# Performance work log

Hardware: AMD Instinct MI355X
Metric: run time of the kernel (lower is better)

## Reference

```python
import jax, jax.numpy as jnp
import numpy as np

C = 16          # state channels
RATE = 0.5      # stochastic update rate
PI2 = 6.283185307179586


def _perception_kernel():
    # depthwise 3x3x3 filters: identity + sobel along each spatial axis
    g = np.array([1.0, 2.0, 1.0], np.float32)
    d = np.array([-1.0, 0.0, 1.0], np.float32)
    ident = np.zeros((3, 3, 3), np.float32); ident[1, 1, 1] = 1.0
    sx = np.einsum('i,j,k->ijk', d, g, g) / 8.0
    sy = np.einsum('i,j,k->ijk', g, d, g) / 8.0
    sz = np.einsum('i,j,k->ijk', g, g, d) / 8.0
    filt = np.stack([ident, sx, sy, sz])                 # [4,3,3,3]
    k = np.broadcast_to(filt, (C, 4, 3, 3, 3)).reshape(C * 4, 1, 3, 3, 3)
    return jnp.asarray(k)                                # [4C,1,3,3,3] OIDHW, groups=C


def _forward(x, rand_u, w1, b1, w2):
    # alive mask: 3x3x3 max-pool (stride 1, SAME) on alpha channel 3, > 0.1
    alpha = x[:, 3:4]
    pooled = jax.lax.reduce_window(alpha, -jnp.inf, jax.lax.max,
                                   (1, 1, 3, 3, 3), (1, 1, 1, 1, 1), 'SAME')
    alive = (pooled > 0.1).astype(x.dtype)               # [B,1,D,H,W]

    # anisotropic perception: depthwise stencil -> [B,4C,D,H,W]
    p = jax.lax.conv_general_dilated(
        x, _perception_kernel(), window_strides=(1, 1, 1), padding='SAME',
        dimension_numbers=('NCDHW', 'OIDHW', 'NCDHW'), feature_group_count=C)

    # per-voxel MLP (1x1x1 convs): 4C -> hidden -> C
    h = jax.nn.relu(jnp.einsum('bcxyz,oc->boxyz', p, w1)
                    + b1[None, :, None, None, None])
    upd = jnp.einsum('bcxyz,oc->boxyz', h, w2)

    # stochastic residual update + alive gating (ANISOTROPIC: 0 orientation ch.)
    smask = (rand_u <= RATE).astype(x.dtype)             # [B,1,D,H,W]
    x = x + upd * smask
    return x * alive


def setup_inputs() -> dict:
    key = jax.random.key(0)
    k1, k2, k3, k4, k5 = jax.random.split(key, 5)
    B, D = 4, 64
    H, P = 128, 4 * C
    x = jax.random.normal(k1, (B, C, D, D, D), jnp.float32)
    rand_u = jax.random.uniform(k2, (B, 1, D, D, D), jnp.float32)
    w1 = jax.random.normal(k3, (H, P), jnp.float32) * (1.0 / np.sqrt(P))
    b1 = jax.random.normal(k4, (H,), jnp.float32) * 0.01
    w2 = jax.random.normal(k5, (C, H), jnp.float32) * (1.0 / np.sqrt(H))
    return {"x": x, "rand_u": rand_u, "w1": w1, "b1": b1, "w2": w2}


def reference(x, rand_u, w1, b1, w2):
    return _forward(x, rand_u, w1, b1, w2)
```

## Files before the change

### kernel.cpp

```cpp
#include <hip/hip_runtime.h>

#define QST 600
#define NSITES 2400


typedef __attribute__((ext_vector_type(8))) short bf16x8;
typedef __attribute__((ext_vector_type(4))) float f32x4;
typedef __attribute__((ext_vector_type(2))) float f32x2;

__device__ __forceinline__ unsigned short f2bf(float f) {
    __bf16 h = (__bf16)f;
    return __builtin_bit_cast(unsigned short, h);
}
__device__ __forceinline__ unsigned packbf2(float lo, float hi) {
    return (unsigned)f2bf(lo) | ((unsigned)f2bf(hi) << 16);
}
__device__ __forceinline__ float blo(unsigned u) { return __builtin_bit_cast(float, u << 16); }
__device__ __forceinline__ float bhi(unsigned u) { return __builtin_bit_cast(float, u & 0xffff0000u); }
__device__ __forceinline__ bf16x8 pack8f(const float* s, const float* scl) {
    bf16x8 o;
    #pragma unroll
    for (int k = 0; k < 8; ++k) o[k] = (short)f2bf(s[k] * scl[k & 3]);
    return o;
}

__global__ __launch_bounds__(256) void permute_w(
    const float* __restrict__ w1, const float* __restrict__ w2,
    unsigned short* __restrict__ wsW)
{
    const int t = threadIdx.x;
    const float sclW1[4] = {1.f, 0.125f, 0.125f, 0.125f};
    const float sclId[4] = {1.f, 1.f, 1.f, 1.f};
    #pragma unroll
    for (int j = 0; j < 4; ++j) {
        int w = t + 256 * j;
        int lane = w & 63, f = (w >> 6) & 3, ch = w >> 8;
        int r16 = lane & 15, g = lane >> 4;
        int row = ch * 32 + 8 * (r16 >> 2) + (r16 & 3) + 4 * (f >> 1);
        int col = (f & 1) * 32 + g * 8;
        *(bf16x8*)(wsW + w * 8) = pack8f(w1 + row * 64 + col, sclW1);
    }
    {
        int w = t;
        int lane = w & 63, ch = w >> 6;
        int r16 = lane & 15, g = lane >> 4;
        *(bf16x8*)(wsW + 8192 + w * 8) = pack8f(w2 + r16 * 128 + ch * 32 + g * 8, sclId);
    }
}

__global__ __launch_bounds__(256, 3) void nca_fused(
    const float* __restrict__ x, const float* __restrict__ rand_u,
    const unsigned short* __restrict__ wsW, const float* __restrict__ b1,
    float* __restrict__ out)
{
    __shared__ __align__(16) char smem[51968];
    uint2*          tq = (uint2*)smem;
    unsigned short* Ps = (unsigned short*)(smem + 19200);

    const int tid = threadIdx.x;

    const int orig = blockIdx.x + 8 * blockIdx.y + 64 * blockIdx.z;
    const int work = (orig & 7) * 512 + (orig >> 3);
    const int gx0 = (work & 7) * 8;
    const int gy0 = ((work >> 3) & 7) * 8;
    const int zb  = work >> 6;
    const int b   = zb >> 4, gz0 = (zb & 15) * 4;
    const int xbase = b * (16 * 262144);

    const int tx = tid & 7, ty = (tid >> 3) & 7, tz = tid >> 6;

    const float ru = rand_u[b * 262144 + (gz0 + tz) * 4096 + (gy0 + ty) * 64 + (gx0 + tx)];

    if (tid < 240) {
        int cq = tid / 60, rem = tid - cq * 60;
        int z = rem / 10, y = rem - z * 10;
        int gz = gz0 + z - 1, gy = gy0 + y - 1;
        uint4* dst = (uint4*)(tq + cq * QST + z * 100 + y * 10);
        if ((unsigned)gz < 64u && (unsigned)gy < 64u) {
            const bool lok = (gx0 > 0), rok = (gx0 < 56);
            const float* base = x + xbase + cq * (4 * 262144) + gz * 4096 + gy * 64 + gx0;
            float va[10], vb[10];
            unsigned wlo[10], whi[10];
            #pragma unroll
            for (int half = 0; half < 2; ++half) {
                #pragma unroll
                for (int cc = 0; cc < 2; ++cc) {
                    const float* bp = base + (2 * half + cc) * 262144;
                    float* v = cc ? vb : va;
                    float4 a4 = *(const float4*)(bp);
                    float4 b4 = *(const float4*)(bp + 4);
                    v[0] = lok ? bp[-1] : 0.f;
                    v[1] = a4.x; v[2] = a4.y; v[3] = a4.z; v[4] = a4.w;
                    v[5] = b4.x; v[6] = b4.y; v[7] = b4.z; v[8] = b4.w;
                    v[9] = rok ? bp[8] : 0.f;
                }
                unsigned* wdst = half ? whi : wlo;
                #pragma unroll
                for (int k = 0; k < 10; ++k) wdst[k] = packbf2(va[k], vb[k]);
            }
            #pragma unroll
            for (int k = 0; k < 5; ++k)
                dst[k] = make_uint4(wlo[2 * k], whi[2 * k], wlo[2 * k + 1], whi[2 * k + 1]);
        } else {
            #pragma unroll
            for (int k = 0; k < 5; ++k)
                dst[k] = make_uint4(0u, 0u, 0u, 0u);
        }
    }
    __syncthreads();

    const int lane = tid & 63, wv = tid >> 6;
    const int g = lane >> 4, r16 = lane & 15;
    const int rowbase = (tz * 10 + ty) * 10 + tx;

    float pool3 = -1e30f;
    const f32x2 two = 2.f;

    #pragma unroll
    for (int cq = 0; cq < 4; ++cq) {
        uint2 q[3][3][3];
        #pragma unroll
        for (int i2 = 0; i2 < 3; ++i2)
            #pragma unroll
            for (int j = 0; j < 3; ++j) {
                const uint2* rp = tq + cq * QST + i2 * 100 + j * 10 + rowbase;
                q[i2][j][0] = rp[0]; q[i2][j][1] = rp[1]; q[i2][j][2] = rp[2];
            }

        f32x2 s1p[2], s2p[2], s3p[2];
        uint2 idq = q[1][1][1];
        #pragma unroll
        for (int pr = 0; pr < 2; ++pr) { s1p[pr] = 0.f; s2p[pr] = 0.f; s3p[pr] = 0.f; }

        #pragma unroll
        for (int i2 = 0; i2 < 3; ++i2) {
            f32x2 Ap[2], Bp[2], Cp[2];
            #pragma unroll
            for (int pr = 0; pr < 2; ++pr) { Ap[pr] = 0.f; Bp[pr] = 0.f; Cp[pr] = 0.f; }
            #pragma unroll
            for (int j = 0; j < 3; ++j) {
                uint2 q0 = q[i2][j][0], q1 = q[i2][j][1], q2 = q[i2][j][2];
                f32x2 v0[2] = { {blo(q0.x), bhi(q0.x)}, {blo(q0.y), bhi(q0.y)} };
                f32x2 v1[2] = { {blo(q1.x), bhi(q1.x)}, {blo(q1.y), bhi(q1.y)} };
                f32x2 v2[2] = { {blo(q2.x), bhi(q2.x)}, {blo(q2.y), bhi(q2.y)} };
                if (cq == 0)
                    pool3 = fmaxf(pool3, fmaxf(fmaxf(v0[1].y, v1[1].y), v2[1].y));
                #pragma unroll
                for (int pr = 0; pr < 2; ++pr) {
                    f32x2 rg = __builtin_elementwise_fma(two, v1[pr], v0[pr] + v2[pr]);
                    f32x2 rd = v2[pr] - v0[pr];
                    if (j == 1) {
                        Ap[pr] = __builtin_elementwise_fma(two, rg, Ap[pr]);
                        Cp[pr] = __builtin_elementwise_fma(two, rd, Cp[pr]);
                    } else {
                        Ap[pr] = Ap[pr] + rg;
                        Cp[pr] = Cp[pr] + rd;
                        if (j == 0) Bp[pr] = Bp[pr] - rg;
                        else        Bp[pr] = Bp[pr] + rg;
                    }
                }
            }
            #pragma unroll
            for (int pr = 0; pr < 2; ++pr) {
                if (i2 == 0) {
                    s1p[pr] = s1p[pr] - Ap[pr];
                    s2p[pr] = s2p[pr] + Bp[pr];
                    s3p[pr] = s3p[pr] + Cp[pr];
                } else if (i2 == 1) {
                    s2p[pr] = __builtin_elementwise_fma(two, Bp[pr], s2p[pr]);
                    s3p[pr] = __builtin_elementwise_fma(two, Cp[pr], s3p[pr]);
                } else {
                    s1p[pr] = s1p[pr] + Ap[pr];
                    s2p[pr] = s2p[pr] + Bp[pr];
                    s3p[pr] = s3p[pr] + Cp[pr];
                }
            }
        }
        unsigned short ide[4] = {
            (unsigned short)(idq.x & 0xffffu), (unsigned short)(idq.x >> 16),
            (unsigned short)(idq.y & 0xffffu), (unsigned short)(idq.y >> 16) };
        float s1e[4] = { s1p[0].x, s1p[0].y, s1p[1].x, s1p[1].y };
        float s2e[4] = { s2p[0].x, s2p[0].y, s2p[1].x, s2p[1].y };
        float s3e[4] = { s3p[0].x, s3p[0].y, s3p[1].x, s3p[1].y };
        unsigned pk8[8];
        #pragma unroll
        for (int e = 0; e < 4; ++e) {
            pk8[2 * e]     = (unsigned)ide[e] | ((unsigned)f2bf(s1e[e]) << 16);
            pk8[2 * e + 1] = packbf2(s2e[e], s3e[e]);
        }
        int s0 = (2 * cq)     ^ (tid & 7);
        int s1 = (2 * cq + 1) ^ (tid & 7);
        *(uint4*)(smem + 19200 + tid * 128 + s0 * 16) = make_uint4(pk8[0], pk8[1], pk8[2], pk8[3]);
        *(uint4*)(smem + 19200 + tid * 128 + s1 * 16) = make_uint4(pk8[4], pk8[5], pk8[6], pk8[7]);
    }
    int mpack = (pool3 > 0.1f) ? ((ru <= 0.5f) ? 3 : 1) : 0;

    asm volatile("s_waitcnt lgkmcnt(0)" ::: "memory");
    __builtin_amdgcn_sched_barrier(0);

    bf16x8 pf[4][2];
    #pragma unroll
    for (int n = 0; n < 4; ++n) {
        int v = (4 * wv + n) * 16 + r16;
        #pragma unroll
        for (int ks = 0; ks < 2; ++ks) {
            int sl = (ks * 4 + g) ^ (r16 & 7);
            pf[n][ks] = *(const bf16x8*)(Ps + v * 64 + sl * 8);
        }
    }

    f32x4 acc2[4] = {{0,0,0,0},{0,0,0,0},{0,0,0,0},{0,0,0,0}};
    const f32x4 z4 = {0,0,0,0};

    #pragma unroll
    for (int ch = 0; ch < 4; ++ch) {
        const bf16x8 aE0 = *(const bf16x8*)(wsW + ((ch * 4 + 0) * 64 + lane) * 8);
        const bf16x8 aE1 = *(const bf16x8*)(wsW + ((ch * 4 + 1) * 64 + lane) * 8);
        const bf16x8 aO0 = *(const bf16x8*)(wsW + ((ch * 4 + 2) * 64 + lane) * 8);
        const bf16x8 aO1 = *(const bf16x8*)(wsW + ((ch * 4 + 3) * 64 + lane) * 8);
        const bf16x8 w2f = *(const bf16x8*)(wsW + 8192 + (ch * 64 + lane) * 8);
        const float4 bE4 = *(const float4*)(b1 + ch * 32 + 8 * g);
        const float4 bO4 = *(const float4*)(b1 + ch * 32 + 8 * g + 4);
        const f32x4 cE = {bE4.x, bE4.y, bE4.z, bE4.w};
        const f32x4 cO = {bO4.x, bO4.y, bO4.z, bO4.w};

        #pragma unroll
        for (int n = 0; n < 4; ++n) {
            f32x4 accE, accO;
            accE = __builtin_amdgcn_mfma_f32_16x16x32_bf16(aE0, pf[n][0], cE, 0, 0, 0);
            accE = __builtin_amdgcn_mfma_f32_16x16x32_bf16(aE1, pf[n][1], accE, 0, 0, 0);
            accO = __builtin_amdgcn_mfma_f32_16x16x32_bf16(aO0, pf[n][0], cO, 0, 0, 0);
            accO = __builtin_amdgcn_mfma_f32_16x16x32_bf16(aO1, pf[n][1], accO, 0, 0, 0);
            f32x4 mE = __builtin_elementwise_max(accE, z4);
            f32x4 mO = __builtin_elementwise_max(accO, z4);
            bf16x8 hb;
            hb[0] = (short)f2bf(mE[0]); hb[1] = (short)f2bf(mE[1]);
            hb[2] = (short)f2bf(mE[2]); hb[3] = (short)f2bf(mE[3]);
            hb[4] = (short)f2bf(mO[0]); hb[5] = (short)f2bf(mO[1]);
            hb[6] = (short)f2bf(mO[2]); hb[7] = (short)f2bf(mO[3]);
            acc2[n] = __builtin_amdgcn_mfma_f32_16x16x32_bf16(w2f, hb, acc2[n], 0, 0, 0);
        }
    }

    #pragma unroll
    for (int n = 0; n < 4; ++n) {
        int v = (4 * wv + n) * 16 + r16;
        int mb = __shfl(mpack, 16 * n + r16, 64);
        float al = (float)(mb & 1), mu = (float)(mb >> 1);
        int vx = v & 7, vy = (v >> 3) & 7;
        int gidx = xbase + (gz0 + wv) * 4096 + (gy0 + vy) * 64 + (gx0 + vx);
        #pragma unroll
        for (int reg = 0; reg < 4; ++reg) {
            int c = 4 * g + reg;
            int sl = (2 * g + (reg >> 1)) ^ (r16 & 7);
            unsigned short cs = Ps[v * 64 + sl * 8 + 4 * (reg & 1)];
            float xc = __builtin_bit_cast(float, (unsigned)cs << 16);
            out[gidx + c * 262144] = xc * al + acc2[n][reg] * mu;
        }
    }
}

extern "C" void kernel_launch(void* const* d_in, const int* in_sizes, int n_in,
                              void* d_out, int out_size, void* d_ws, size_t ws_size,
                              hipStream_t stream)
{
    const float* x      = (const float*)d_in[0];
    const float* rand_u = (const float*)d_in[1];
    const float* w1     = (const float*)d_in[2];
    const float* b1     = (const float*)d_in[3];
    const float* w2     = (const float*)d_in[4];
    float* out = (float*)d_out;
    unsigned short* wsW = (unsigned short*)d_ws;

    permute_w<<<dim3(1), dim3(256), 0, stream>>>(w1, w2, wsW);

    dim3 grid(8, 8, 64);
    dim3 block(256);
    nca_fused<<<grid, block, 0, stream>>>(x, rand_u, wsW, b1, out);
}
```

Baseline: 81.50 us.

## Halve perception LDS buffer via two-phase staging to raise occupancy

Perception features are now written to shared memory in two halves, each read back into MFMA fragments before the next half overwrites it. This cuts the LDS footprint from about 52KB to about 35KB and raises launch bounds from 3 to 4 blocks per CU. The w2 rows are permuted so the residual identity channels can be taken from the already-loaded fragments instead of re-reading LDS. The cost is an extra wait and sched barrier per phase and possibly more register pressure under the tighter bound.

```diff
diff --git a/kernel.cpp b/kernel.cpp
--- a/kernel.cpp
+++ b/kernel.cpp
@@ -2,6 +2,7 @@
 
 #define QST 600
 #define NSITES 2400
+#define PH_OFF 19200
 
 
 typedef __attribute__((ext_vector_type(8))) short bf16x8;
@@ -44,18 +45,19 @@
         int w = t;
         int lane = w & 63, ch = w >> 6;
         int r16 = lane & 15, g = lane >> 4;
-        *(bf16x8*)(wsW + 8192 + w * 8) = pack8f(w2 + r16 * 128 + ch * 32 + g * 8, sclId);
-    }
-}
-
-__global__ __launch_bounds__(256, 3) void nca_fused(
+        int ch2 = 2 * (r16 >> 2) + (r16 & 1) + 8 * ((r16 >> 1) & 1);
+        *(bf16x8*)(wsW + 8192 + w * 8) = pack8f(w2 + ch2 * 128 + ch * 32 + g * 8, sclId);
+    }
+}
+
+__global__ __launch_bounds__(256, 4) void nca_fused(
     const float* __restrict__ x, const float* __restrict__ rand_u,
     const unsigned short* __restrict__ wsW, const float* __restrict__ b1,
     float* __restrict__ out)
 {
-    __shared__ __align__(16) char smem[51968];
+    __shared__ __align__(16) char smem[35584];
     uint2*          tq = (uint2*)smem;
-    unsigned short* Ps = (unsigned short*)(smem + 19200);
+    unsigned short* Ph = (unsigned short*)(smem + PH_OFF);
 
     const int tid = threadIdx.x;
 
@@ -112,102 +114,105 @@
     const int lane = tid & 63, wv = tid >> 6;
     const int g = lane >> 4, r16 = lane & 15;
     const int rowbase = (tz * 10 + ty) * 10 + tx;
+    const int sw = (tid >> 1) & 3;
 
     float pool3 = -1e30f;
     const f32x2 two = 2.f;
-
-    #pragma unroll
-    for (int cq = 0; cq < 4; ++cq) {
-        uint2 q[3][3][3];
-        #pragma unroll
-        for (int i2 = 0; i2 < 3; ++i2)
-            #pragma unroll
-            for (int j = 0; j < 3; ++j) {
-                const uint2* rp = tq + cq * QST + i2 * 100 + j * 10 + rowbase;
-                q[i2][j][0] = rp[0]; q[i2][j][1] = rp[1]; q[i2][j][2] = rp[2];
+    bf16x8 pf[4][2];
+
+    #pragma unroll
+    for (int ph = 0; ph < 2; ++ph) {
+        #pragma unroll
+        for (int ch2 = 0; ch2 < 2; ++ch2) {
+            const int cq = 2 * ph + ch2;
+            uint2 q[3][3][3];
+            #pragma unroll
+            for (int i2 = 0; i2 < 3; ++i2)
+                #pragma unroll
+                for (int j = 0; j < 3; ++j) {
+                    const uint2* rp = tq + cq * QST + i2 * 100 + j * 10 + rowbase;
+                    q[i2][j][0] = rp[0]; q[i2][j][1] = rp[1]; q[i2][j][2] = rp[2];
+                }
+
+            f32x2 s1p[2], s2p[2], s3p[2];
+            uint2 idq = q[1][1][1];
+            #pragma unroll
+            for (int pr = 0; pr < 2; ++pr) { s1p[pr] = 0.f; s2p[pr] = 0.f; s3p[pr] = 0.f; }
+
+            #pragma unroll
+            for (int i2 = 0; i2 < 3; ++i2) {
+                f32x2 Ap[2], Bp[2], Cp[2];
+                #pragma unroll
+                for (int pr = 0; pr < 2; ++pr) { Ap[pr] = 0.f; Bp[pr] = 0.f; Cp[pr] = 0.f; }
+                #pragma unroll
+                for (int j = 0; j < 3; ++j) {
+                    uint2 q0 = q[i2][j][0], q1 = q[i2][j][1], q2 = q[i2][j][2];
+                    f32x2 v0[2] = { {blo(q0.x), bhi(q0.x)}, {blo(q0.y), bhi(q0.y)} };
+                    f32x2 v1[2] = { {blo(q1.x), bhi(q1.x)}, {blo(q1.y), bhi(q1.y)} };
+                    f32x2 v2[2] = { {blo(q2.x), bhi(q2.x)}, {blo(q2.y), bhi(q2.y)} };
+                    if (cq == 0)
+                        pool3 = fmaxf(pool3, fmaxf(fmaxf(v0[1].y, v1[1].y), v2[1].y));
+                    #pragma unroll
+                    for (int pr = 0; pr < 2; ++pr) {
+                        f32x2 rg = __builtin_elementwise_fma(two, v1[pr], v0[pr] + v2[pr]);
+                        f32x2 rd = v2[pr] - v0[pr];
+                        if (j == 1) {
+                            Ap[pr] = __builtin_elementwise_fma(two, rg, Ap[pr]);
+                            Cp[pr] = __builtin_elementwise_fma(two, rd, Cp[pr]);
+                        } else {
+                            Ap[pr] = Ap[pr] + rg;
+                            Cp[pr] = Cp[pr] + rd;
+                            if (j == 0) Bp[pr] = Bp[pr] - rg;
+                            else        Bp[pr] = Bp[pr] + rg;
+                        }
+                    }
+                }
+                #pragma unroll
+                for (int pr = 0; pr < 2; ++pr) {
+                    if (i2 == 0) {
+                        s1p[pr] = s1p[pr] - Ap[pr];
+                        s2p[pr] = s2p[pr] + Bp[pr];
+                        s3p[pr] = s3p[pr] + Cp[pr];
+                    } else if (i2 == 1) {
+                        s2p[pr] = __builtin_elementwise_fma(two, Bp[pr], s2p[pr]);
+                        s3p[pr] = __builtin_elementwise_fma(two, Cp[pr], s3p[pr]);
+                    } else {
+                        s1p[pr] = s1p[pr] + Ap[pr];
+                        s2p[pr] = s2p[pr] + Bp[pr];
+                        s3p[pr] = s3p[pr] + Cp[pr];
+                    }
+                }
             }
-
-        f32x2 s1p[2], s2p[2], s3p[2];
-        uint2 idq = q[1][1][1];
-        #pragma unroll
-        for (int pr = 0; pr < 2; ++pr) { s1p[pr] = 0.f; s2p[pr] = 0.f; s3p[pr] = 0.f; }
-
-        #pragma unroll
-        for (int i2 = 0; i2 < 3; ++i2) {
-            f32x2 Ap[2], Bp[2], Cp[2];
-            #pragma unroll
-            for (int pr = 0; pr < 2; ++pr) { Ap[pr] = 0.f; Bp[pr] = 0.f; Cp[pr] = 0.f; }
-            #pragma unroll
-            for (int j = 0; j < 3; ++j) {
-                uint2 q0 = q[i2][j][0], q1 = q[i2][j][1], q2 = q[i2][j][2];
-                f32x2 v0[2] = { {blo(q0.x), bhi(q0.x)}, {blo(q0.y), bhi(q0.y)} };
-                f32x2 v1[2] = { {blo(q1.x), bhi(q1.x)}, {blo(q1.y), bhi(q1.y)} };
-                f32x2 v2[2] = { {blo(q2.x), bhi(q2.x)}, {blo(q2.y), bhi(q2.y)} };
-                if (cq == 0)
-                    pool3 = fmaxf(pool3, fmaxf(fmaxf(v0[1].y, v1[1].y), v2[1].y));
-                #pragma unroll
-                for (int pr = 0; pr < 2; ++pr) {
-                    f32x2 rg = __builtin_elementwise_fma(two, v1[pr], v0[pr] + v2[pr]);
-                    f32x2 rd = v2[pr] - v0[pr];
-                    if (j == 1) {
-                        Ap[pr] = __builtin_elementwise_fma(two, rg, Ap[pr]);
-                        Cp[pr] = __builtin_elementwise_fma(two, rd, Cp[pr]);
-                    } else {
-                        Ap[pr] = Ap[pr] + rg;
-                        Cp[pr] = Cp[pr] + rd;
-                        if (j == 0) Bp[pr] = Bp[pr] - rg;
-                        else        Bp[pr] = Bp[pr] + rg;
-                    }
-                }
+            unsigned short ide[4] = {
+                (unsigned short)(idq.x & 0xffffu), (unsigned short)(idq.x >> 16),
+                (unsigned short)(idq.y & 0xffffu), (unsigned short)(idq.y >> 16) };
+            float s1e[4] = { s1p[0].x, s1p[0].y, s1p[1].x, s1p[1].y };
+            float s2e[4] = { s2p[0].x, s2p[0].y, s2p[1].x, s2p[1].y };
+            float s3e[4] = { s3p[0].x, s3p[0].y, s3p[1].x, s3p[1].y };
+            unsigned pk8[8];
+            #pragma unroll
+            for (int e = 0; e < 4; ++e) {
+                pk8[2 * e]     = (unsigned)ide[e] | ((unsigned)f2bf(s1e[e]) << 16);
+                pk8[2 * e + 1] = packbf2(s2e[e], s3e[e]);
             }
-            #pragma unroll
-            for (int pr = 0; pr < 2; ++pr) {
-                if (i2 == 0) {
-                    s1p[pr] = s1p[pr] - Ap[pr];
-                    s2p[pr] = s2p[pr] + Bp[pr];
-                    s3p[pr] = s3p[pr] + Cp[pr];
-                } else if (i2 == 1) {
-                    s2p[pr] = __builtin_elementwise_fma(two, Bp[pr], s2p[pr]);
-                    s3p[pr] = __builtin_elementwise_fma(two, Cp[pr], s3p[pr]);
-                } else {
-                    s1p[pr] = s1p[pr] + Ap[pr];
-                    s2p[pr] = s2p[pr] + Bp[pr];
-                    s3p[pr] = s3p[pr] + Cp[pr];
-                }
-            }
-        }
-        unsigned short ide[4] = {
-            (unsigned short)(idq.x & 0xffffu), (unsigned short)(idq.x >> 16),
-            (unsigned short)(idq.y & 0xffffu), (unsigned short)(idq.y >> 16) };
-        float s1e[4] = { s1p[0].x, s1p[0].y, s1p[1].x, s1p[1].y };
-        float s2e[4] = { s2p[0].x, s2p[0].y, s2p[1].x, s2p[1].y };
-        float s3e[4] = { s3p[0].x, s3p[0].y, s3p[1].x, s3p[1].y };
-        unsigned pk8[8];
-        #pragma unroll
-        for (int e = 0; e < 4; ++e) {
-            pk8[2 * e]     = (unsigned)ide[e] | ((unsigned)f2bf(s1e[e]) << 16);
-            pk8[2 * e + 1] = packbf2(s2e[e], s3e[e]);
-        }
-        int s0 = (2 * cq)     ^ (tid & 7);
-        int s1 = (2 * cq + 1) ^ (tid & 7);
-        *(uint4*)(smem + 19200 + tid * 128 + s0 * 16) = make_uint4(pk8[0], pk8[1], pk8[2], pk8[3]);
-        *(uint4*)(smem + 19200 + tid * 128 + s1 * 16) = make_uint4(pk8[4], pk8[5], pk8[6], pk8[7]);
+            int s0 = (2 * ch2)     ^ sw;
+            int s1 = (2 * ch2 + 1) ^ sw;
+            *(uint4*)(smem + PH_OFF + tid * 64 + s0 * 16) = make_uint4(pk8[0], pk8[1], pk8[2], pk8[3]);
+            *(uint4*)(smem + PH_OFF + tid * 64 + s1 * 16) = make_uint4(pk8[4], pk8[5], pk8[6], pk8[7]);
+        }
+
+        asm volatile("s_waitcnt lgkmcnt(0)" ::: "memory");
+        __builtin_amdgcn_sched_barrier(0);
+        #pragma unroll
+        for (int n = 0; n < 4; ++n) {
+            int v = (4 * wv + n) * 16 + r16;
+            int sl = g ^ ((v >> 1) & 3);
+            pf[n][ph] = *(const bf16x8*)(Ph + v * 32 + sl * 8);
+        }
+        asm volatile("s_waitcnt lgkmcnt(0)" ::: "memory");
+        __builtin_amdgcn_sched_barrier(0);
     }
     int mpack = (pool3 > 0.1f) ? ((ru <= 0.5f) ? 3 : 1) : 0;
-
-    asm volatile("s_waitcnt lgkmcnt(0)" ::: "memory");
-    __builtin_amdgcn_sched_barrier(0);
-
-    bf16x8 pf[4][2];
-    #pragma unroll
-    for (int n = 0; n < 4; ++n) {
-        int v = (4 * wv + n) * 16 + r16;
-        #pragma unroll
-        for (int ks = 0; ks < 2; ++ks) {
-            int sl = (ks * 4 + g) ^ (r16 & 7);
-            pf[n][ks] = *(const bf16x8*)(Ps + v * 64 + sl * 8);
-        }
-    }
 
     f32x4 acc2[4] = {{0,0,0,0},{0,0,0,0},{0,0,0,0},{0,0,0,0}};
     const f32x4 z4 = {0,0,0,0};
@@ -251,9 +256,8 @@
         int gidx = xbase + (gz0 + wv) * 4096 + (gy0 + vy) * 64 + (gx0 + vx);
         #pragma unroll
         for (int reg = 0; reg < 4; ++reg) {
-            int c = 4 * g + reg;
-            int sl = (2 * g + (reg >> 1)) ^ (r16 & 7);
-            unsigned short cs = Ps[v * 64 + sl * 8 + 4 * (reg & 1)];
+            int c = 2 * g + (reg & 1) + 8 * (reg >> 1);
+            unsigned short cs = (unsigned short)pf[n][reg >> 1][(reg & 1) * 4];
             float xc = __builtin_bit_cast(float, (unsigned)cs << 16);
             out[gidx + c * 262144] = xc * al + acc2[n][reg] * mu;
         }
```

Result: slower. 115.6 us (+41.8%).
